# Kernel optimization log

Hardware: AMD Instinct MI355X
Metric: run time of the kernel (lower is better)

## Reference

```python
import jax, jax.numpy as jnp
import numpy as np

HEADS = 8
KS = 4      # kernel_size
ST = 2      # stride


def setup_inputs() -> dict:
    key = jax.random.key(0)
    k1, k2, k3, k4 = jax.random.split(key, 4)
    B, L, C = 8, 2048, 1024
    s = C ** -0.5  # keep projections O(1) so softmax logits don't saturate
    x = jax.random.normal(k1, (B, L, C), dtype=jnp.float32)
    w_qkv = jax.random.normal(k2, (C, 3 * C), dtype=jnp.float32) * s
    w_out = jax.random.normal(k3, (C, C), dtype=jnp.float32) * s
    b_out = jax.random.normal(k4, (C,), dtype=jnp.float32)
    return {"x": x, "w_qkv": w_qkv, "w_out": w_out, "b_out": b_out}


def reference(x, w_qkv, w_out, b_out):
    B, L, C = x.shape
    H = HEADS
    Dh = C // H
    scale = C ** -0.5  # NOTE: original scales by full dim, not head dim

    # QKV once for all tokens (windows are slices, so this equals per-window proj)
    qkv = x @ w_qkv                                    # [B, L, 3C]

    # window start indices: i in range(0, L-KS+1, ST)
    starts = jnp.arange(0, L - KS + 1, ST)             # [N]
    idx = starts[:, None] + jnp.arange(KS)[None, :]    # [N, KS]

    win = qkv[:, idx]                                  # [B, N, KS, 3C]
    q, k, v = jnp.split(win, 3, axis=-1)               # each [B, N, KS, C]
    N = starts.shape[0]
    q = q.reshape(B, N, KS, H, Dh)
    k = k.reshape(B, N, KS, H, Dh)
    v = v.reshape(B, N, KS, H, Dh)

    dots = jnp.einsum("bnqhd,bnkhd->bnhqk", q, k) * scale  # [B,N,H,KS,KS]
    attn = jax.nn.softmax(dots, axis=-1)
    o = jnp.einsum("bnhqk,bnkhd->bnqhd", attn, v)          # [B,N,KS,H,Dh]
    o = o.reshape(B, N, KS, C)

    y = o @ w_out + b_out                               # per-window to_out [B,N,KS,C]

    # overlap-add accumulation into the output
    out = jnp.zeros((B, L, C), dtype=x.dtype)
    out = out.at[:, idx.reshape(-1), :].add(y.reshape(B, N * KS, C))
    return out
```

## Files before the change

kernel.cpp:

```cpp
#include <hip/hip_runtime.h>
#include <stdint.h>

#define HEADS 8
#define KSZ   4
#define STRD  2
#define BB    8
#define LL    2048
#define CC    1024
#define N3    3072
#define NW    1023
#define M1    (BB*LL)
#define GK    1024
#define NTT   16

typedef __bf16 bf16;
typedef __bf16 bf16x8 __attribute__((ext_vector_type(8)));
typedef float  f32x4  __attribute__((ext_vector_type(4)));
typedef unsigned int  u32;
typedef unsigned short u16;

__device__ __forceinline__ float bflo(u32 u) { return __uint_as_float(u << 16); }
__device__ __forceinline__ float bfhi(u32 u) { return __uint_as_float(u & 0xffff0000u); }
__device__ __forceinline__ u16 f2bf(float f) { bf16 b = (bf16)f; return __builtin_bit_cast(u16, b); }

#define AS3(p) ((__attribute__((address_space(3))) void*)(p))
#define AS1(p) ((const __attribute__((address_space(1))) void*)(p))

__device__ __forceinline__ void tr_block(const float* __restrict__ src,
                                         bf16* __restrict__ dst,
                                         int R, int Ccol, int c0, int r0)
{
    __shared__ float t[32][33];
    int tx = threadIdx.x & 31, ty = threadIdx.x >> 5;
#pragma unroll
    for (int yy = 0; yy < 32; yy += 8)
        t[ty + yy][tx] = src[(size_t)(r0 + ty + yy) * Ccol + c0 + tx];
    __syncthreads();
#pragma unroll
    for (int yy = 0; yy < 32; yy += 8)
        dst[(size_t)(c0 + ty + yy) * R + r0 + tx] = (bf16)t[tx][ty + yy];
}

__global__ __launch_bounds__(256) void prep_k(const float* __restrict__ x,
                                              bf16* __restrict__ xb,
                                              const float* __restrict__ w_qkv,
                                              bf16* __restrict__ wqkvT,
                                              const float* __restrict__ w_out,
                                              bf16* __restrict__ woutT)
{
    int bid = blockIdx.x;
    if (bid < 2048) {
        const int n4 = M1 * CC / 4;
        int i = bid * 256 + threadIdx.x;
        for (; i < n4; i += 2048 * 256) {
            float4 f = reinterpret_cast<const float4*>(x)[i];
            ushort4 u;
            u.x = f2bf(f.x); u.y = f2bf(f.y); u.z = f2bf(f.z); u.w = f2bf(f.w);
            reinterpret_cast<ushort4*>(xb)[i] = u;
        }
    } else if (bid < 5120) {
        int t = bid - 2048;
        tr_block(w_qkv, wqkvT, CC, N3, (t % 96) * 32, (t / 96) * 32);
    } else {
        int t = bid - 5120;
        tr_block(w_out, woutT, CC, CC, (t & 31) * 32, (t >> 5) * 32);
    }
}

__device__ __forceinline__ void stage8(const bf16* __restrict__ G, bf16* dst,
                                       int baserow, int kt,
                                       int wid, int l, int kch)
{
#pragma unroll
    for (int qd = 0; qd < 4; ++qd) {
        int row = ((wid * 4 + qd) << 3) + (l >> 3);
        const bf16* src = G + (size_t)(baserow + row) * GK + kt * 64 + kch;
        __builtin_amdgcn_global_load_lds(AS1(src), AS3(dst + (wid * 4 + qd) * 512), 16, 0, 0);
    }
}

template <int OUT_MODE, int T, int NBN>
__global__ __launch_bounds__(512, 1) void gemm8p_k(const bf16* __restrict__ A,
                                                   const bf16* __restrict__ Bt,
                                                   void* __restrict__ Cout,
                                                   const float* __restrict__ bias)
{
    __shared__ __attribute__((aligned(16))) bf16 sA[2][256 * 64];
    __shared__ __attribute__((aligned(16))) bf16 sB[2][256 * 64];
    const int Nn = NBN << 8;

    const int tid = threadIdx.x;
    const int l = tid & 63, wid = tid >> 6;
    const int wm = wid >> 2, wn = wid & 3;
    const int l15 = l & 15, l4 = l >> 4;
    const int xr = (l & 7) << 4;
    const int kch = ((l & 7) ^ ((l >> 3) & 7)) * 8;

    const int nwg = gridDim.x;
    const int wg = ((blockIdx.x & 7) * (nwg >> 3)) + (blockIdx.x >> 3);
    const int JT = T * NTT;

    int ti = wg * T;
    int m0 = (ti / NBN) << 8, n0 = (ti % NBN) << 8;

    const int rA = wm * 128 + l15;
    const int rB = wn * 64 + l15;
    int offK[2];
#pragma unroll
    for (int ks = 0; ks < 2; ++ks)
        offK[ks] = ((ks * 64 + l4 * 16) ^ xr) >> 1;

    f32x4 acc[8][4] = {};
    bf16x8 aLo[4][2], aHi[4][2], bLo[2][2], bHi[2][2];

    stage8(A, sA[0], m0, 0, wid, l, kch);
    stage8(Bt, sB[0], n0, 0, wid, l, kch);
    stage8(A, sA[1], m0, 1, wid, l, kch);
    stage8(Bt, sB[1], n0, 1, wid, l, kch);
    asm volatile("s_waitcnt vmcnt(8)" ::: "memory");
    __builtin_amdgcn_s_barrier();
    __builtin_amdgcn_sched_barrier(0);

    for (int j = 0; j < JT; ++j) {
        const bf16* tA = sA[j & 1];
        const bf16* tB = sB[j & 1];
        bf16* wA = sA[j & 1];
        bf16* wB = sB[j & 1];

        const int jn = j + 2;
        const bool doStage = jn < JT;
        int ktn = jn & (NTT - 1), m0n = 0, n0n = 0;
        if (doStage) {
            int tin = wg * T + (jn >> 4);
            m0n = (tin / NBN) << 8;
            n0n = (tin % NBN) << 8;
        }

#pragma unroll
        for (int m = 0; m < 4; ++m)
#pragma unroll
            for (int ks = 0; ks < 2; ++ks)
                aLo[m][ks] = *reinterpret_cast<const bf16x8*>(&tA[(rA + m * 16) * 64 + offK[ks]]);
#pragma unroll
        for (int n = 0; n < 2; ++n)
#pragma unroll
            for (int ks = 0; ks < 2; ++ks)
                bLo[n][ks] = *reinterpret_cast<const bf16x8*>(&tB[(rB + n * 16) * 64 + offK[ks]]);
        __builtin_amdgcn_s_setprio(1);
#pragma unroll
        for (int m = 0; m < 4; ++m)
#pragma unroll
            for (int n = 0; n < 2; ++n)
#pragma unroll
                for (int ks = 0; ks < 2; ++ks)
                    acc[m][n] = __builtin_amdgcn_mfma_f32_16x16x32_bf16(aLo[m][ks], bLo[n][ks], acc[m][n], 0, 0, 0);
        __builtin_amdgcn_s_setprio(0);
        __builtin_amdgcn_s_barrier();
        __builtin_amdgcn_sched_barrier(0);

#pragma unroll
        for (int m = 0; m < 4; ++m)
#pragma unroll
            for (int ks = 0; ks < 2; ++ks)
                aHi[m][ks] = *reinterpret_cast<const bf16x8*>(&tA[(rA + 64 + m * 16) * 64 + offK[ks]]);
        __builtin_amdgcn_s_setprio(1);
#pragma unroll
        for (int m = 0; m < 4; ++m)
#pragma unroll
            for (int n = 0; n < 2; ++n)
#pragma unroll
                for (int ks = 0; ks < 2; ++ks)
                    acc[4 + m][n] = __builtin_amdgcn_mfma_f32_16x16x32_bf16(aHi[m][ks], bLo[n][ks], acc[4 + m][n], 0, 0, 0);
        __builtin_amdgcn_s_setprio(0);
        __builtin_amdgcn_s_barrier();
        __builtin_amdgcn_sched_barrier(0);

#pragma unroll
        for (int n = 0; n < 2; ++n)
#pragma unroll
            for (int ks = 0; ks < 2; ++ks)
                bHi[n][ks] = *reinterpret_cast<const bf16x8*>(&tB[(rB + 32 + n * 16) * 64 + offK[ks]]);
        if (doStage)
            stage8(A, wA, m0n, ktn, wid, l, kch);
        __builtin_amdgcn_s_setprio(1);
#pragma unroll
        for (int m = 0; m < 4; ++m)
#pragma unroll
            for (int n = 0; n < 2; ++n)
#pragma unroll
                for (int ks = 0; ks < 2; ++ks)
                    acc[4 + m][2 + n] = __builtin_amdgcn_mfma_f32_16x16x32_bf16(aHi[m][ks], bHi[n][ks], acc[4 + m][2 + n], 0, 0, 0);
        __builtin_amdgcn_s_setprio(0);
        __builtin_amdgcn_s_barrier();
        __builtin_amdgcn_sched_barrier(0);

        if (doStage)
            stage8(Bt, wB, n0n, ktn, wid, l, kch);
        __builtin_amdgcn_s_setprio(1);
#pragma unroll
        for (int m = 0; m < 4; ++m)
#pragma unroll
            for (int n = 0; n < 2; ++n)
#pragma unroll
                for (int ks = 0; ks < 2; ++ks)
                    acc[m][2 + n] = __builtin_amdgcn_mfma_f32_16x16x32_bf16(aLo[m][ks], bHi[n][ks], acc[m][2 + n], 0, 0, 0);
        __builtin_amdgcn_s_setprio(0);
        if (j < JT - 2)
            asm volatile("s_waitcnt vmcnt(8)" ::: "memory");
        else if (j == JT - 2)
            asm volatile("s_waitcnt vmcnt(0)" ::: "memory");
        __builtin_amdgcn_s_barrier();
        __builtin_amdgcn_sched_barrier(0);

        if ((j & (NTT - 1)) == NTT - 1) {
            if (OUT_MODE == 0) {
                bf16* Cb = (bf16*)Cout;
#pragma unroll
                for (int m = 0; m < 8; ++m) {
                    int row = m0 + wm * 128 + m * 16 + l4 * 4;
#pragma unroll
                    for (int n = 0; n < 4; ++n) {
                        int col = n0 + wn * 64 + n * 16 + l15;
#pragma unroll
                        for (int r = 0; r < 4; ++r)
                            Cb[(size_t)(row + r) * Nn + col] = (bf16)acc[m][n][r];
                    }
                }
            } else {
                float* Cf = (float*)Cout;
#pragma unroll
                for (int m = 0; m < 8; ++m) {
                    int row = m0 + wm * 128 + m * 16 + l4 * 4;
#pragma unroll
                    for (int n = 0; n < 4; ++n) {
                        int col = n0 + wn * 64 + n * 16 + l15;
                        float bv = bias[col];
#pragma unroll
                        for (int r = 0; r < 4; ++r) {
                            int lrow = (row + r) & (LL - 1);
                            float cnt = (lrow < 2 || lrow > LL - 3) ? 1.f : 2.f;
                            Cf[(size_t)(row + r) * Nn + col] = acc[m][n][r] + bv * cnt;
                        }
                    }
                }
            }
            if (j + 1 < JT) {
#pragma unroll
                for (int m = 0; m < 8; ++m)
#pragma unroll
                    for (int n = 0; n < 4; ++n)
#pragma unroll
                        for (int r = 0; r < 4; ++r)
                            acc[m][n][r] = 0.f;
                ti += 1;
                m0 = (ti / NBN) << 8;
                n0 = (ti % NBN) << 8;
            }
        }
    }
}

__global__ __launch_bounds__(256) void attnz4_k(const bf16* __restrict__ qkv,
                                                bf16* __restrict__ z)
{
    int bid = (blockIdx.x & 7) * 512 + (blockIdx.x >> 3);
    int task = bid * 4 + (threadIdx.x >> 6);
    int h = task & 7;
    int tmp = task >> 3;
    int p = tmp & 255;
    int b = tmp >> 8;
    int l = threadIdx.x & 63;
    const int coff = h * 128 + 2 * l;
    const int browz = b * LL + 8 * p;

    float q[8][2], k[12][2], v[12][2];
#pragma unroll
    for (int i = 0; i < 8; ++i) {
        const bf16* rp = qkv + (size_t)(browz + i) * N3;
        u32 uq = *reinterpret_cast<const u32*>(rp + coff);
        q[i][0] = bflo(uq); q[i][1] = bfhi(uq);
    }
#pragma unroll
    for (int s = 0; s < 12; ++s) {
        int r = 8 * p - 2 + s;
        r = r < 0 ? 0 : (r > LL - 1 ? LL - 1 : r);
        const bf16* rp = qkv + (size_t)(b * LL + r) * N3;
        u32 uk = *reinterpret_cast<const u32*>(rp + 1024 + coff);
        u32 uv = *reinterpret_cast<const u32*>(rp + 2048 + coff);
        k[s][0] = bflo(uk); k[s][1] = bfhi(uk);
        v[s][0] = bflo(uv); v[s][1] = bfhi(uv);
    }

    float dots[8][6];
#pragma unroll
    for (int i = 0; i < 8; ++i) {
        const int base = (i >> 1) << 1;
#pragma unroll
        for (int j = 0; j < 6; ++j) {
            float pp = q[i][0] * k[base + j][0] + q[i][1] * k[base + j][1];
#pragma unroll
            for (int off = 32; off >= 1; off >>= 1)
                pp += __shfl_xor(pp, off);
            dots[i][j] = pp * 0.03125f;
        }
    }

#pragma unroll
    for (int i = 0; i < 8; ++i) {
        const int base = (i >> 1) << 1;
        const bool cLo = !(p == 0 && i < 2);
        const bool cHi = !(p == 255 && i >= 6);
        float o0 = 0.f, o1 = 0.f;
        if (cLo) {
            float m = fmaxf(fmaxf(dots[i][0], dots[i][1]), fmaxf(dots[i][2], dots[i][3]));
            float e[4], s = 0.f;
#pragma unroll
            for (int j = 0; j < 4; ++j) { e[j] = __expf(dots[i][j] - m); s += e[j]; }
            float inv = 1.f / s;
#pragma unroll
            for (int j = 0; j < 4; ++j) {
                float a = e[j] * inv;
                o0 += a * v[base + j][0];
                o1 += a * v[base + j][1];
            }
        }
        if (cHi) {
            float m = fmaxf(fmaxf(dots[i][2], dots[i][3]), fmaxf(dots[i][4], dots[i][5]));
            float e[4], s = 0.f;
#pragma unroll
            for (int j = 0; j < 4; ++j) { e[j] = __expf(dots[i][2 + j] - m); s += e[j]; }
            float inv = 1.f / s;
#pragma unroll
            for (int j = 0; j < 4; ++j) {
                float a = e[j] * inv;
                o0 += a * v[base + 2 + j][0];
                o1 += a * v[base + 2 + j][1];
            }
        }
        u32 pk = (u32)f2bf(o0) | ((u32)f2bf(o1) << 16);
        *reinterpret_cast<u32*>(z + (size_t)(browz + i) * CC + coff) = pk;
    }
}

extern "C" void kernel_launch(void* const* d_in, const int* in_sizes, int n_in,
                              void* d_out, int out_size, void* d_ws, size_t ws_size,
                              hipStream_t stream)
{
    const float* x     = (const float*)d_in[0];
    const float* w_qkv = (const float*)d_in[1];
    const float* w_out = (const float*)d_in[2];
    const float* b_out = (const float*)d_in[3];
    float* out = (float*)d_out;
    char* ws = (char*)d_ws;

    bf16* xb    = (bf16*)(ws);
    bf16* wqkvT = (bf16*)(ws + 33554432);
    bf16* woutT = (bf16*)(ws + 39845888);
    bf16* qkvb  = (bf16*)(ws + 41943040);
    bf16* z     = (bf16*)(ws + 142606336);

    prep_k<<<6144, 256, 0, stream>>>(x, xb, w_qkv, wqkvT, w_out, woutT);

    gemm8p_k<0, 3, 12><<<256, 512, 0, stream>>>(xb, wqkvT, qkvb, nullptr);

    attnz4_k<<<4096, 256, 0, stream>>>(qkvb, z);

    gemm8p_k<1, 1, 4><<<256, 512, 0, stream>>>(z, woutT, out, b_out);
}
```

Before: 227.3 us.

## Shrink GEMM tiles to 128x256 with K=32 steps for higher occupancy

Replaces the 256x256 tile, K=64 double-buffered GEMM with a 128x256 tile, K=32 variant that uses much less LDS and fewer accumulator registers, allowing several workgroups per CU (launch bounds 4). The grid doubles to 512 workgroups, the LDS swizzle is adapted to 32-wide rows, and the pipeline drops from four barrier phases to two per k-step. The goal is better latency hiding through occupancy, at the cost of lower per-tile data reuse, more barriers per unit of work and more global traffic.

New measurement: 234.8 us. 3.3% more time.

```diff
diff --git a/kernel.cpp b/kernel.cpp
--- a/kernel.cpp
+++ b/kernel.cpp
@@ -11,7 +11,7 @@
 #define NW    1023
 #define M1    (BB*LL)
 #define GK    1024
-#define NTT   16
+#define NT2   32
 
 typedef __bf16 bf16;
 typedef __bf16 bf16x8 __attribute__((ext_vector_type(8)));
@@ -67,57 +67,62 @@
     }
 }
 
-__device__ __forceinline__ void stage8(const bf16* __restrict__ G, bf16* dst,
-                                       int baserow, int kt,
-                                       int wid, int l, int kch)
-{
-#pragma unroll
-    for (int qd = 0; qd < 4; ++qd) {
-        int row = ((wid * 4 + qd) << 3) + (l >> 3);
-        const bf16* src = G + (size_t)(baserow + row) * GK + kt * 64 + kch;
-        __builtin_amdgcn_global_load_lds(AS1(src), AS3(dst + (wid * 4 + qd) * 512), 16, 0, 0);
+__device__ __forceinline__ void stageA2(const bf16* __restrict__ G, bf16* dst,
+                                        int baserow, int kt, int wid, int l)
+{
+    int c = wid * 64 + l;
+    int row = c >> 2;
+    int kc = (c & 3) ^ ((row >> 1) & 3);
+    const bf16* src = G + (size_t)(baserow + row) * GK + kt * 32 + kc * 8;
+    __builtin_amdgcn_global_load_lds(AS1(src), AS3(dst + wid * 512), 16, 0, 0);
+}
+__device__ __forceinline__ void stageB2(const bf16* __restrict__ G, bf16* dst,
+                                        int baserow, int kt, int wid, int l)
+{
+#pragma unroll
+    for (int i = 0; i < 2; ++i) {
+        int c = i * 512 + wid * 64 + l;
+        int row = c >> 2;
+        int kc = (c & 3) ^ ((row >> 1) & 3);
+        const bf16* src = G + (size_t)(baserow + row) * GK + kt * 32 + kc * 8;
+        __builtin_amdgcn_global_load_lds(AS1(src), AS3(dst + (i * 512 + wid * 64) * 8), 16, 0, 0);
     }
 }
 
 template <int OUT_MODE, int T, int NBN>
-__global__ __launch_bounds__(512, 1) void gemm8p_k(const bf16* __restrict__ A,
+__global__ __launch_bounds__(512, 4) void gemm2p_k(const bf16* __restrict__ A,
                                                    const bf16* __restrict__ Bt,
                                                    void* __restrict__ Cout,
                                                    const float* __restrict__ bias)
 {
-    __shared__ __attribute__((aligned(16))) bf16 sA[2][256 * 64];
-    __shared__ __attribute__((aligned(16))) bf16 sB[2][256 * 64];
+    __shared__ __attribute__((aligned(16))) bf16 sA[2][128 * 32];
+    __shared__ __attribute__((aligned(16))) bf16 sB[2][256 * 32];
     const int Nn = NBN << 8;
 
     const int tid = threadIdx.x;
     const int l = tid & 63, wid = tid >> 6;
     const int wm = wid >> 2, wn = wid & 3;
-    const int l15 = l & 15, l4 = l >> 4;
-    const int xr = (l & 7) << 4;
-    const int kch = ((l & 7) ^ ((l >> 3) & 7)) * 8;
+    const int l15 = l & 15, l4 = (l >> 4) & 3;
+    const int offE = (l4 ^ ((l15 >> 1) & 3)) << 3;
 
     const int nwg = gridDim.x;
     const int wg = ((blockIdx.x & 7) * (nwg >> 3)) + (blockIdx.x >> 3);
-    const int JT = T * NTT;
+    const int JT = T * NT2;
 
     int ti = wg * T;
-    int m0 = (ti / NBN) << 8, n0 = (ti % NBN) << 8;
-
-    const int rA = wm * 128 + l15;
+    int m0 = (ti / NBN) << 7, n0 = (ti % NBN) << 8;
+
+    const int rA = wm * 64 + l15;
     const int rB = wn * 64 + l15;
-    int offK[2];
-#pragma unroll
-    for (int ks = 0; ks < 2; ++ks)
-        offK[ks] = ((ks * 64 + l4 * 16) ^ xr) >> 1;
-
-    f32x4 acc[8][4] = {};
-    bf16x8 aLo[4][2], aHi[4][2], bLo[2][2], bHi[2][2];
-
-    stage8(A, sA[0], m0, 0, wid, l, kch);
-    stage8(Bt, sB[0], n0, 0, wid, l, kch);
-    stage8(A, sA[1], m0, 1, wid, l, kch);
-    stage8(Bt, sB[1], n0, 1, wid, l, kch);
-    asm volatile("s_waitcnt vmcnt(8)" ::: "memory");
+
+    f32x4 acc[4][4] = {};
+    bf16x8 a[4], b[4];
+
+    stageA2(A, sA[0], m0, 0, wid, l);
+    stageB2(Bt, sB[0], n0, 0, wid, l);
+    stageA2(A, sA[1], m0, 1, wid, l);
+    stageB2(Bt, sB[1], n0, 1, wid, l);
+    asm volatile("s_waitcnt vmcnt(3)" ::: "memory");
     __builtin_amdgcn_s_barrier();
     __builtin_amdgcn_sched_barrier(0);
 
@@ -129,131 +134,91 @@
 
         const int jn = j + 2;
         const bool doStage = jn < JT;
-        int ktn = jn & (NTT - 1), m0n = 0, n0n = 0;
+        int ktn = jn & (NT2 - 1), m0n = 0, n0n = 0;
         if (doStage) {
-            int tin = wg * T + (jn >> 4);
-            m0n = (tin / NBN) << 8;
+            int tin = wg * T + (jn >> 5);
+            m0n = (tin / NBN) << 7;
             n0n = (tin % NBN) << 8;
         }
 
 #pragma unroll
+        for (int f = 0; f < 4; ++f)
+            a[f] = *reinterpret_cast<const bf16x8*>(&tA[(rA + f * 16) * 32 + offE]);
+#pragma unroll
+        for (int f = 0; f < 4; ++f)
+            b[f] = *reinterpret_cast<const bf16x8*>(&tB[(rB + f * 16) * 32 + offE]);
+        __builtin_amdgcn_s_setprio(1);
+#pragma unroll
         for (int m = 0; m < 4; ++m)
 #pragma unroll
-            for (int ks = 0; ks < 2; ++ks)
-                aLo[m][ks] = *reinterpret_cast<const bf16x8*>(&tA[(rA + m * 16) * 64 + offK[ks]]);
-#pragma unroll
-        for (int n = 0; n < 2; ++n)
-#pragma unroll
-            for (int ks = 0; ks < 2; ++ks)
-                bLo[n][ks] = *reinterpret_cast<const bf16x8*>(&tB[(rB + n * 16) * 64 + offK[ks]]);
-        __builtin_amdgcn_s_setprio(1);
-#pragma unroll
-        for (int m = 0; m < 4; ++m)
-#pragma unroll
             for (int n = 0; n < 2; ++n)
-#pragma unroll
-                for (int ks = 0; ks < 2; ++ks)
-                    acc[m][n] = __builtin_amdgcn_mfma_f32_16x16x32_bf16(aLo[m][ks], bLo[n][ks], acc[m][n], 0, 0, 0);
+                acc[m][n] = __builtin_amdgcn_mfma_f32_16x16x32_bf16(a[m], b[n], acc[m][n], 0, 0, 0);
         __builtin_amdgcn_s_setprio(0);
+        asm volatile("s_waitcnt lgkmcnt(0)" ::: "memory");
+        __builtin_amdgcn_sched_barrier(0);
         __builtin_amdgcn_s_barrier();
         __builtin_amdgcn_sched_barrier(0);
 
+        if (doStage) {
+            stageA2(A, wA, m0n, ktn, wid, l);
+            stageB2(Bt, wB, n0n, ktn, wid, l);
+        }
+        __builtin_amdgcn_s_setprio(1);
 #pragma unroll
         for (int m = 0; m < 4; ++m)
 #pragma unroll
-            for (int ks = 0; ks < 2; ++ks)
-                aHi[m][ks] = *reinterpret_cast<const bf16x8*>(&tA[(rA + 64 + m * 16) * 64 + offK[ks]]);
-        __builtin_amdgcn_s_setprio(1);
-#pragma unroll
-        for (int m = 0; m < 4; ++m)
-#pragma unroll
             for (int n = 0; n < 2; ++n)
-#pragma unroll
-                for (int ks = 0; ks < 2; ++ks)
-                    acc[4 + m][n] = __builtin_amdgcn_mfma_f32_16x16x32_bf16(aHi[m][ks], bLo[n][ks], acc[4 + m][n], 0, 0, 0);
-        __builtin_amdgcn_s_setprio(0);
-        __builtin_amdgcn_s_barrier();
-        __builtin_amdgcn_sched_barrier(0);
-
-#pragma unroll
-        for (int n = 0; n < 2; ++n)
-#pragma unroll
-            for (int ks = 0; ks < 2; ++ks)
-                bHi[n][ks] = *reinterpret_cast<const bf16x8*>(&tB[(rB + 32 + n * 16) * 64 + offK[ks]]);
-        if (doStage)
-            stage8(A, wA, m0n, ktn, wid, l, kch);
-        __builtin_amdgcn_s_setprio(1);
-#pragma unroll
-        for (int m = 0; m < 4; ++m)
-#pragma unroll
-            for (int n = 0; n < 2; ++n)
-#pragma unroll
-                for (int ks = 0; ks < 2; ++ks)
-                    acc[4 + m][2 + n] = __builtin_amdgcn_mfma_f32_16x16x32_bf16(aHi[m][ks], bHi[n][ks], acc[4 + m][2 + n], 0, 0, 0);
-        __builtin_amdgcn_s_setprio(0);
-        __builtin_amdgcn_s_barrier();
-        __builtin_amdgcn_sched_barrier(0);
-
-        if (doStage)
-            stage8(Bt, wB, n0n, ktn, wid, l, kch);
-        __builtin_amdgcn_s_setprio(1);
-#pragma unroll
-        for (int m = 0; m < 4; ++m)
-#pragma unroll
-            for (int n = 0; n < 2; ++n)
-#pragma unroll
-                for (int ks = 0; ks < 2; ++ks)
-                    acc[m][2 + n] = __builtin_amdgcn_mfma_f32_16x16x32_bf16(aLo[m][ks], bHi[n][ks], acc[m][2 + n], 0, 0, 0);
+                acc[m][2 + n] = __builtin_amdgcn_mfma_f32_16x16x32_bf16(a[m], b[2 + n], acc[m][2 + n], 0, 0, 0);
         __builtin_amdgcn_s_setprio(0);
         if (j < JT - 2)
-            asm volatile("s_waitcnt vmcnt(8)" ::: "memory");
+            asm volatile("s_waitcnt vmcnt(3)" ::: "memory");
         else if (j == JT - 2)
             asm volatile("s_waitcnt vmcnt(0)" ::: "memory");
         __builtin_amdgcn_s_barrier();
         __builtin_amdgcn_sched_barrier(0);
 
-        if ((j & (NTT - 1)) == NTT - 1) {
+        if ((j & (NT2 - 1)) == NT2 - 1) {
             if (OUT_MODE == 0) {
                 bf16* Cb = (bf16*)Cout;
 #pragma unroll
-                for (int m = 0; m < 8; ++m) {
-                    int row = m0 + wm * 128 + m * 16 + l4 * 4;
-#pragma unroll
-                    for (int n = 0; n < 4; ++n) {
-                        int col = n0 + wn * 64 + n * 16 + l15;
+                for (int mf = 0; mf < 4; ++mf) {
+                    int row = m0 + wm * 64 + mf * 16 + l4 * 4;
+#pragma unroll
+                    for (int nf = 0; nf < 4; ++nf) {
+                        int col = n0 + wn * 64 + nf * 16 + l15;
 #pragma unroll
                         for (int r = 0; r < 4; ++r)
-                            Cb[(size_t)(row + r) * Nn + col] = (bf16)acc[m][n][r];
+                            Cb[(size_t)(row + r) * Nn + col] = (bf16)acc[mf][nf][r];
                     }
                 }
             } else {
                 float* Cf = (float*)Cout;
 #pragma unroll
-                for (int m = 0; m < 8; ++m) {
-                    int row = m0 + wm * 128 + m * 16 + l4 * 4;
-#pragma unroll
-                    for (int n = 0; n < 4; ++n) {
-                        int col = n0 + wn * 64 + n * 16 + l15;
+                for (int mf = 0; mf < 4; ++mf) {
+                    int row = m0 + wm * 64 + mf * 16 + l4 * 4;
+#pragma unroll
+                    for (int nf = 0; nf < 4; ++nf) {
+                        int col = n0 + wn * 64 + nf * 16 + l15;
                         float bv = bias[col];
 #pragma unroll
                         for (int r = 0; r < 4; ++r) {
                             int lrow = (row + r) & (LL - 1);
                             float cnt = (lrow < 2 || lrow > LL - 3) ? 1.f : 2.f;
-                            Cf[(size_t)(row + r) * Nn + col] = acc[m][n][r] + bv * cnt;
+                            Cf[(size_t)(row + r) * Nn + col] = acc[mf][nf][r] + bv * cnt;
                         }
                     }
                 }
             }
             if (j + 1 < JT) {
 #pragma unroll
-                for (int m = 0; m < 8; ++m)
-#pragma unroll
-                    for (int n = 0; n < 4; ++n)
+                for (int mf = 0; mf < 4; ++mf)
+#pragma unroll
+                    for (int nf = 0; nf < 4; ++nf)
 #pragma unroll
                         for (int r = 0; r < 4; ++r)
-                            acc[m][n][r] = 0.f;
+                            acc[mf][nf][r] = 0.f;
                 ti += 1;
-                m0 = (ti / NBN) << 8;
+                m0 = (ti / NBN) << 7;
                 n0 = (ti % NBN) << 8;
             }
         }
@@ -319,9 +284,9 @@
             float inv = 1.f / s;
 #pragma unroll
             for (int j = 0; j < 4; ++j) {
-                float a = e[j] * inv;
-                o0 += a * v[base + j][0];
-                o1 += a * v[base + j][1];
+                float aa = e[j] * inv;
+                o0 += aa * v[base + j][0];
+                o1 += aa * v[base + j][1];
             }
         }
         if (cHi) {
@@ -332,9 +297,9 @@
             float inv = 1.f / s;
 #pragma unroll
             for (int j = 0; j < 4; ++j) {
-                float a = e[j] * inv;
-                o0 += a * v[base + 2 + j][0];
-                o1 += a * v[base + 2 + j][1];
+                float aa = e[j] * inv;
+                o0 += aa * v[base + 2 + j][0];
+                o1 += aa * v[base + 2 + j][1];
             }
         }
         u32 pk = (u32)f2bf(o0) | ((u32)f2bf(o1) << 16);
@@ -361,9 +326,9 @@
 
     prep_k<<<6144, 256, 0, stream>>>(x, xb, w_qkv, wqkvT, w_out, woutT);
 
-    gemm8p_k<0, 3, 12><<<256, 512, 0, stream>>>(xb, wqkvT, qkvb, nullptr);
+    gemm2p_k<0, 3, 12><<<512, 512, 0, stream>>>(xb, wqkvT, qkvb, nullptr);
 
     attnz4_k<<<4096, 256, 0, stream>>>(qkvb, z);
 
-    gemm8p_k<1, 1, 4><<<256, 512, 0, stream>>>(z, woutT, out, b_out);
-}
+    gemm2p_k<1, 1, 4><<<512, 512, 0, stream>>>(z, woutT, out, b_out);
+}
```
